# Kernel tuning notes

Hardware: AMD Instinct MI355X
Metric: run time of the kernel (lower is better)

The kernel has to match this reference:

```python
import jax, jax.numpy as jnp
import numpy as np

B, S, H = 32, 2048, 1024
STDV = 0.1


def setup_inputs() -> dict:
    key = jax.random.key(0)
    ks = jax.random.split(key, 8)
    u = lambda k, shape: jax.random.uniform(k, shape, minval=-STDV, maxval=STDV, dtype=jnp.float32)
    return {
        "inputs": jax.random.normal(ks[0], (B, S, H), dtype=jnp.float32),
        "qvector": jax.random.normal(ks[1], (B, H), dtype=jnp.float32),
        "W_u_1": u(ks[2], (H, H)),
        "W_u_m_1": u(ks[3], (H, H)),
        "W_u_h_1": u(ks[4], (H, 1)),
        "W_u_2": u(ks[5], (H, H)),
        "W_u_m_2": u(ks[6], (H, H)),
        "W_u_h_2": u(ks[7], (H, 1)),
    }


def reference(inputs, qvector, W_u_1, W_u_m_1, W_u_h_1, W_u_2, W_u_m_2, W_u_h_2):
    # inputs: [B, S, H], qvector: [B, H]
    def hop(m, W, Wm, Wh):
        # M = tanh(inputs @ W) gated by tanh(m @ Wm)  -> [B, S, H]
        M = jnp.tanh(jnp.einsum("bsh,hd->bsd", inputs, W))
        M = M * jnp.tanh(m @ Wm)[:, None, :]
        U = jnp.einsum("bsd,do->bso", M, Wh)        # [B, S, 1]
        alpha = jax.nn.softmax(U, axis=1)           # softmax over sequence
        return jnp.sum(inputs * alpha, axis=1)      # [B, H]

    mean_in = jnp.mean(inputs, axis=1)              # [B, H]
    u_att0 = mean_in
    m0 = mean_in * qvector
    u_att1 = hop(m0, W_u_1, W_u_m_1, W_u_h_1)
    m1 = m0 + u_att0 * qvector
    u_att2 = hop(m1, W_u_2, W_u_m_2, W_u_h_2)
    # original returns list [u_att0, u_att1, u_att2]; stack for a single array
    return jnp.stack([u_att0, u_att1, u_att2])      # [3, B, H]
```

## Files before the change

### kernel.cpp

```cpp
#include <hip/hip_runtime.h>
#include <hip/hip_bf16.h>
#include <math.h>

#define B_  32
#define S_  2048
#define H_  1024
#define M_TOT (B_ * S_)

typedef __bf16 bf16x8 __attribute__((ext_vector_type(8)));
typedef float  f32x4  __attribute__((ext_vector_type(4)));

__device__ __forceinline__ unsigned short f2bf(float f) {
    union { float f; unsigned int u; } v; v.f = f;
    unsigned int u = v.u;
    return (unsigned short)((u + 0x7fffu + ((u >> 16) & 1u)) >> 16);
}

__device__ __forceinline__ float bf2f(unsigned short s) {
    return __uint_as_float(((unsigned int)s) << 16);
}

__device__ __forceinline__ float fast_tanh(float x) {
    float e = __expf(2.0f * x);
    return 1.0f - 2.0f / (e + 1.0f);
}

__global__ void k_meanconv(const float* __restrict__ x,
                           unsigned short* __restrict__ xbf,
                           float* __restrict__ meanOut ) {
    int b  = blockIdx.x;
    int sc = blockIdx.y;
    int t  = threadIdx.x;
    size_t base = ((size_t)b * S_ + (size_t)sc * 32) * H_;
    const float4* xr = (const float4*)(x + base);
    ushort4* xo = (ushort4*)(xbf + base);
    float a0 = 0.f, a1 = 0.f, a2 = 0.f, a3 = 0.f;
    for (int s = 0; s < 32; ++s) {
        float4 v = xr[(size_t)s * 256 + t];
        a0 += v.x; a1 += v.y; a2 += v.z; a3 += v.w;
        ushort4 o;
        o.x = f2bf(v.x); o.y = f2bf(v.y); o.z = f2bf(v.z); o.w = f2bf(v.w);
        xo[(size_t)s * 256 + t] = o;
    }
    const float scl = 1.0f / (float)S_;
    float* mp = meanOut + b * H_ + t * 4;
    atomicAdd(mp + 0, a0 * scl);
    atomicAdd(mp + 1, a1 * scl);
    atomicAdd(mp + 2, a2 * scl);
    atomicAdd(mp + 3, a3 * scl);
}

__global__ void k_wconv(const float* __restrict__ W1,
                        const float* __restrict__ W2,
                        unsigned short* __restrict__ WT) {
    int n = blockIdx.x;
    int t = threadIdx.x;
    const float* src = (n < H_) ? (W1 + n) : (W2 + (n - H_));
    unsigned short* dst = WT + (size_t)n * H_;
    for (int kk = 0; kk < 4; ++kk) {
        int k = t + kk * 256;
        dst[k] = f2bf(src[(size_t)k * H_]);
    }
}

__global__ void k_vpart(const float* __restrict__ meanIn,
                        const float* __restrict__ q,
                        const float* __restrict__ Wm1,
                        const float* __restrict__ Wm2,
                        float* __restrict__ vtmp ) {
    int b   = blockIdx.x;
    int hop = blockIdx.y;
    int hc  = blockIdx.z;
    int t   = threadIdx.x;
    __shared__ float mL[128];
    float scale = (hop == 0) ? 1.0f : 2.0f;
    int h0 = hc * 128;
    if (t < 128)
        mL[t] = meanIn[b * H_ + h0 + t] * q[b * H_ + h0 + t] * scale;
    __syncthreads();
    const float* Wm = hop ? Wm2 : Wm1;
    int d0 = t * 4;
    float a0 = 0.f, a1 = 0.f, a2 = 0.f, a3 = 0.f;
    for (int h = 0; h < 128; ++h) {
        float m = mL[h];
        float4 w = *(const float4*)(Wm + (size_t)(h0 + h) * H_ + d0);
        a0 += m * w.x; a1 += m * w.y; a2 += m * w.z; a3 += m * w.w;
    }
    float* vo = vtmp + b * 2048 + hop * H_ + d0;
    atomicAdd(vo + 0, a0);
    atomicAdd(vo + 1, a1);
    atomicAdd(vo + 2, a2);
    atomicAdd(vo + 3, a3);
}

__global__ void k_vfin(const float* __restrict__ vtmp,
                       const float* __restrict__ Wh1,
                       const float* __restrict__ Wh2,
                       float* __restrict__ vcat) {
    int i = blockIdx.x * 256 + threadIdx.x;
    int hop = (i >> 10) & 1;
    int d = i & 1023;
    const float* Wh = hop ? Wh2 : Wh1;
    vcat[i] = tanhf(vtmp[i]) * Wh[d];
}

__global__ __launch_bounds__(256) void k_gemm(const unsigned short* __restrict__ Xbf,
                                              const unsigned short* __restrict__ WT,
                                              const float* __restrict__ vcat,
                                              float* __restrict__ U ) {
    int nt = blockIdx.x;
    int mt = blockIdx.y;
    int m0 = mt * 128;
    int n0 = nt * 128;
    int t    = threadIdx.x;
    int lane = t & 63;
    int wave = t >> 6;
    int wm = wave >> 1, wn = wave & 1;
    int fr = lane & 15;
    int fq = lane >> 4;

    __shared__ unsigned short As[128 * 32];
    __shared__ unsigned short Bs[128 * 32];

    f32x4 acc[4][4];
#pragma unroll
    for (int i = 0; i < 4; ++i)
#pragma unroll
        for (int j = 0; j < 4; ++j)
#pragma unroll
            for (int r = 0; r < 4; ++r) acc[i][j][r] = 0.0f;

    int idx0 = t, idx1 = t + 256;
    int row0 = idx0 >> 2, kc0 = ((idx0 & 3) - ((row0 >> 1) & 3)) & 3;
    int row1 = idx1 >> 2, kc1 = ((idx1 & 3) - ((row1 >> 1) & 3)) & 3;
    const unsigned short* gA0 = Xbf + (size_t)(m0 + row0) * H_ + kc0 * 8;
    const unsigned short* gA1 = Xbf + (size_t)(m0 + row1) * H_ + kc1 * 8;
    const unsigned short* gB0 = WT  + (size_t)(n0 + row0) * H_ + kc0 * 8;
    const unsigned short* gB1 = WT  + (size_t)(n0 + row1) * H_ + kc1 * 8;
    unsigned short* lA0 = As + idx0 * 8;
    unsigned short* lA1 = As + idx1 * 8;
    unsigned short* lB0 = Bs + idx0 * 8;
    unsigned short* lB1 = Bs + idx1 * 8;

    int slotR = (fq + ((fr >> 1) & 3)) & 3;
    const bf16x8* pa[4];
    const bf16x8* pb[4];
#pragma unroll
    for (int i = 0; i < 4; ++i)
        pa[i] = (const bf16x8*)(As + ((wm * 64 + i * 16 + fr) * 4 + slotR) * 8);
#pragma unroll
    for (int j = 0; j < 4; ++j)
        pb[j] = (const bf16x8*)(Bs + ((wn * 64 + j * 16 + fr) * 4 + slotR) * 8);

    for (int k0 = 0; k0 < H_; k0 += 32) {
        __builtin_amdgcn_global_load_lds((const __attribute__((address_space(1))) void*)(gA0 + k0),
                                         (__attribute__((address_space(3))) void*)lA0, 16, 0, 0);
        __builtin_amdgcn_global_load_lds((const __attribute__((address_space(1))) void*)(gA1 + k0),
                                         (__attribute__((address_space(3))) void*)lA1, 16, 0, 0);
        __builtin_amdgcn_global_load_lds((const __attribute__((address_space(1))) void*)(gB0 + k0),
                                         (__attribute__((address_space(3))) void*)lB0, 16, 0, 0);
        __builtin_amdgcn_global_load_lds((const __attribute__((address_space(1))) void*)(gB1 + k0),
                                         (__attribute__((address_space(3))) void*)lB1, 16, 0, 0);
        __syncthreads();
        bf16x8 af[4], bg[4];
#pragma unroll
        for (int i = 0; i < 4; ++i) af[i] = *pa[i];
#pragma unroll
        for (int j = 0; j < 4; ++j) bg[j] = *pb[j];
#pragma unroll
        for (int i = 0; i < 4; ++i)
#pragma unroll
            for (int j = 0; j < 4; ++j)
                acc[i][j] = __builtin_amdgcn_mfma_f32_16x16x32_bf16(af[i], bg[j], acc[i][j], 0, 0, 0);
        __syncthreads();
    }

    int b   = m0 >> 11;
    int hop = n0 >> 10;
    float vv[4];
#pragma unroll
    for (int j = 0; j < 4; ++j)
        vv[j] = vcat[b * 2048 + n0 + wn * 64 + j * 16 + fr];

#pragma unroll
    for (int i = 0; i < 4; ++i) {
#pragma unroll
        for (int r = 0; r < 4; ++r) {
            float sum = fast_tanh(acc[i][0][r]) * vv[0]
                      + fast_tanh(acc[i][1][r]) * vv[1]
                      + fast_tanh(acc[i][2][r]) * vv[2]
                      + fast_tanh(acc[i][3][r]) * vv[3];
            sum += __shfl_xor(sum, 1);
            sum += __shfl_xor(sum, 2);
            sum += __shfl_xor(sum, 4);
            sum += __shfl_xor(sum, 8);
            if (fr == 0) {
                int row = m0 + wm * 64 + i * 16 + fq * 4 + r;
                atomicAdd(&U[(size_t)hop * M_TOT + row], sum);
            }
        }
    }
}

__global__ void k_softmax(const float* __restrict__ U, float* __restrict__ alpha) {
    int id  = blockIdx.x;
    int hop = id >> 5, b = id & 31;
    int t = threadIdx.x;
    const float* u = U + (size_t)hop * M_TOT + (size_t)b * S_;
    float* al = alpha + (size_t)hop * M_TOT + (size_t)b * S_;
    float v[8];
    float mx = -1e30f;
#pragma unroll
    for (int i = 0; i < 8; ++i) { v[i] = u[t + i * 256]; mx = fmaxf(mx, v[i]); }
    __shared__ float red[256];
    red[t] = mx; __syncthreads();
    for (int s = 128; s > 0; s >>= 1) {
        if (t < s) red[t] = fmaxf(red[t], red[t + s]);
        __syncthreads();
    }
    mx = red[0]; __syncthreads();
    float sum = 0.f;
#pragma unroll
    for (int i = 0; i < 8; ++i) { v[i] = expf(v[i] - mx); sum += v[i]; }
    red[t] = sum; __syncthreads();
    for (int s = 128; s > 0; s >>= 1) {
        if (t < s) red[t] += red[t + s];
        __syncthreads();
    }
    float inv = 1.0f / red[0];
#pragma unroll
    for (int i = 0; i < 8; ++i) al[t + i * 256] = v[i] * inv;
}

__global__ void k_wsum(const unsigned short* __restrict__ Xbf,
                       const float* __restrict__ alpha,
                       float* __restrict__ out1 ,
                       float* __restrict__ out2 ) {
    int b  = blockIdx.x;
    int sc = blockIdx.y;
    int t  = threadIdx.x;
    __shared__ float a1[32], a2[32];
    int s0 = sc * 32;
    if (t < 32)       a1[t]      = alpha[(size_t)b * S_ + s0 + t];
    else if (t < 64)  a2[t - 32] = alpha[(size_t)M_TOT + (size_t)b * S_ + s0 + (t - 32)];
    __syncthreads();
    const ushort4* xr = (const ushort4*)(Xbf + ((size_t)b * S_ + s0) * H_);
    float x0a = 0.f, x1a = 0.f, x2a = 0.f, x3a = 0.f;
    float x0b = 0.f, x1b = 0.f, x2b = 0.f, x3b = 0.f;
    for (int s = 0; s < 32; ++s) {
        ushort4 u = xr[(size_t)s * 256 + t];
        float f0 = bf2f(u.x), f1 = bf2f(u.y), f2 = bf2f(u.z), f3 = bf2f(u.w);
        float w1 = a1[s], w2 = a2[s];
        x0a += f0 * w1; x1a += f1 * w1; x2a += f2 * w1; x3a += f3 * w1;
        x0b += f0 * w2; x1b += f1 * w2; x2b += f2 * w2; x3b += f3 * w2;
    }
    float* o1 = out1 + b * H_ + t * 4;
    float* o2 = out2 + b * H_ + t * 4;
    atomicAdd(o1 + 0, x0a); atomicAdd(o1 + 1, x1a);
    atomicAdd(o1 + 2, x2a); atomicAdd(o1 + 3, x3a);
    atomicAdd(o2 + 0, x0b); atomicAdd(o2 + 1, x1b);
    atomicAdd(o2 + 2, x2b); atomicAdd(o2 + 3, x3b);
}

extern "C" void kernel_launch(void* const* d_in, const int* in_sizes, int n_in,
                              void* d_out, int out_size, void* d_ws, size_t ws_size,
                              hipStream_t stream) {
    const float* inputs = (const float*)d_in[0];
    const float* q      = (const float*)d_in[1];
    const float* W1     = (const float*)d_in[2];
    const float* Wm1    = (const float*)d_in[3];
    const float* Wh1    = (const float*)d_in[4];
    const float* W2     = (const float*)d_in[5];
    const float* Wm2    = (const float*)d_in[6];
    const float* Wh2    = (const float*)d_in[7];
    float* out = (float*)d_out;

    char* ws = (char*)d_ws;
    unsigned short* Xbf  = (unsigned short*)(ws);
    unsigned short* WT   = (unsigned short*)(ws + 134217728);
    float*          vcat = (float*)(ws + 138412032);
    float*          U    = (float*)(ws + 138674176);
    float*          alph = (float*)(ws + 139198464);
    float*          vtmp = (float*)(ws + 139722752);

    hipMemsetAsync(d_out, 0, (size_t)out_size * sizeof(float), stream);
    hipMemsetAsync(U, 0, 524288 + 524288 + 262144, stream);

    k_meanconv<<<dim3(32, 64), 256, 0, stream>>>(inputs, Xbf, out);
    k_wconv  <<<dim3(2048),    256, 0, stream>>>(W1, W2, WT);
    k_vpart  <<<dim3(32, 2, 8), 256, 0, stream>>>(out, q, Wm1, Wm2, vtmp);
    k_vfin   <<<dim3(256),     256, 0, stream>>>(vtmp, Wh1, Wh2, vcat);
    k_gemm   <<<dim3(16, 512), 256, 0, stream>>>(Xbf, WT, vcat, U);
    k_softmax<<<dim3(64),      256, 0, stream>>>(U, alph);
    k_wsum   <<<dim3(32, 64),  256, 0, stream>>>(Xbf, alph, out + 32768, out + 65536);
}
```

Before: 870.0 us.

## Deepen GEMM K-tile to 64, tile weight transpose via LDS, widen wsum loads

The GEMM now stages 64-wide K slices in LDS with an 8-slot XOR-style swizzle, halving the number of barrier pairs per K loop, and adds a launch-bounds occupancy hint. The weight conversion kernel becomes a shared-memory tiled transpose with coalesced float4 reads and ushort4 writes, replacing strided column reads. The weighted-sum kernel uses 8-wide bf16 loads with 128 threads per block. Doubling the LDS footprint and the occupancy hint may cut resident blocks or force register spills.

```diff
diff --git a/kernel.cpp b/kernel.cpp
--- a/kernel.cpp
+++ b/kernel.cpp
@@ -9,6 +9,7 @@
 
 typedef __bf16 bf16x8 __attribute__((ext_vector_type(8)));
 typedef float  f32x4  __attribute__((ext_vector_type(4)));
+typedef unsigned short ushort8 __attribute__((ext_vector_type(8)));
 
 __device__ __forceinline__ unsigned short f2bf(float f) {
     union { float f; unsigned int u; } v; v.f = f;
@@ -53,13 +54,33 @@
 __global__ void k_wconv(const float* __restrict__ W1,
                         const float* __restrict__ W2,
                         unsigned short* __restrict__ WT) {
-    int n = blockIdx.x;
+    __shared__ float tile[64][65];
+    int kt = blockIdx.x * 64;
+    int nt = blockIdx.y * 64;
+    const float* W = blockIdx.z ? W2 : W1;
     int t = threadIdx.x;
-    const float* src = (n < H_) ? (W1 + n) : (W2 + (n - H_));
-    unsigned short* dst = WT + (size_t)n * H_;
-    for (int kk = 0; kk < 4; ++kk) {
-        int k = t + kk * 256;
-        dst[k] = f2bf(src[(size_t)k * H_]);
+    int r  = t >> 4;
+    int c4 = (t & 15) * 4;
+#pragma unroll
+    for (int i = 0; i < 4; ++i) {
+        float4 v = *(const float4*)(W + (size_t)(kt + r + i * 16) * H_ + nt + c4);
+        tile[r + i * 16][c4 + 0] = v.x;
+        tile[r + i * 16][c4 + 1] = v.y;
+        tile[r + i * 16][c4 + 2] = v.z;
+        tile[r + i * 16][c4 + 3] = v.w;
+    }
+    __syncthreads();
+    int n  = t & 63;
+    int kg = (t >> 6) * 16;
+    unsigned short* dst = WT + (size_t)(blockIdx.z * H_ + nt + n) * H_ + kt + kg;
+#pragma unroll
+    for (int jj = 0; jj < 4; ++jj) {
+        ushort4 o;
+        o.x = f2bf(tile[kg + jj * 4 + 0][n]);
+        o.y = f2bf(tile[kg + jj * 4 + 1][n]);
+        o.z = f2bf(tile[kg + jj * 4 + 2][n]);
+        o.w = f2bf(tile[kg + jj * 4 + 3][n]);
+        *(ushort4*)(dst + jj * 4) = o;
     }
 }
 
@@ -104,10 +125,10 @@
     vcat[i] = tanhf(vtmp[i]) * Wh[d];
 }
 
-__global__ __launch_bounds__(256) void k_gemm(const unsigned short* __restrict__ Xbf,
-                                              const unsigned short* __restrict__ WT,
-                                              const float* __restrict__ vcat,
-                                              float* __restrict__ U ) {
+__global__ __launch_bounds__(256, 5) void k_gemm(const unsigned short* __restrict__ Xbf,
+                                                 const unsigned short* __restrict__ WT,
+                                                 const float* __restrict__ vcat,
+                                                 float* __restrict__ U ) {
     int nt = blockIdx.x;
     int mt = blockIdx.y;
     int m0 = mt * 128;
@@ -119,8 +140,8 @@
     int fr = lane & 15;
     int fq = lane >> 4;
 
-    __shared__ unsigned short As[128 * 32];
-    __shared__ unsigned short Bs[128 * 32];
+    __shared__ unsigned short As[128 * 64];
+    __shared__ unsigned short Bs[128 * 64];
 
     f32x4 acc[4][4];
 #pragma unroll
@@ -130,48 +151,56 @@
 #pragma unroll
             for (int r = 0; r < 4; ++r) acc[i][j][r] = 0.0f;
 
-    int idx0 = t, idx1 = t + 256;
-    int row0 = idx0 >> 2, kc0 = ((idx0 & 3) - ((row0 >> 1) & 3)) & 3;
-    int row1 = idx1 >> 2, kc1 = ((idx1 & 3) - ((row1 >> 1) & 3)) & 3;
-    const unsigned short* gA0 = Xbf + (size_t)(m0 + row0) * H_ + kc0 * 8;
-    const unsigned short* gA1 = Xbf + (size_t)(m0 + row1) * H_ + kc1 * 8;
-    const unsigned short* gB0 = WT  + (size_t)(n0 + row0) * H_ + kc0 * 8;
-    const unsigned short* gB1 = WT  + (size_t)(n0 + row1) * H_ + kc1 * 8;
-    unsigned short* lA0 = As + idx0 * 8;
-    unsigned short* lA1 = As + idx1 * 8;
-    unsigned short* lB0 = Bs + idx0 * 8;
-    unsigned short* lB1 = Bs + idx1 * 8;
-
-    int slotR = (fq + ((fr >> 1) & 3)) & 3;
-    const bf16x8* pa[4];
-    const bf16x8* pb[4];
-#pragma unroll
-    for (int i = 0; i < 4; ++i)
-        pa[i] = (const bf16x8*)(As + ((wm * 64 + i * 16 + fr) * 4 + slotR) * 8);
-#pragma unroll
-    for (int j = 0; j < 4; ++j)
-        pb[j] = (const bf16x8*)(Bs + ((wn * 64 + j * 16 + fr) * 4 + slotR) * 8);
-
-    for (int k0 = 0; k0 < H_; k0 += 32) {
-        __builtin_amdgcn_global_load_lds((const __attribute__((address_space(1))) void*)(gA0 + k0),
-                                         (__attribute__((address_space(3))) void*)lA0, 16, 0, 0);
-        __builtin_amdgcn_global_load_lds((const __attribute__((address_space(1))) void*)(gA1 + k0),
-                                         (__attribute__((address_space(3))) void*)lA1, 16, 0, 0);
-        __builtin_amdgcn_global_load_lds((const __attribute__((address_space(1))) void*)(gB0 + k0),
-                                         (__attribute__((address_space(3))) void*)lB0, 16, 0, 0);
-        __builtin_amdgcn_global_load_lds((const __attribute__((address_space(1))) void*)(gB1 + k0),
-                                         (__attribute__((address_space(3))) void*)lB1, 16, 0, 0);
+    const unsigned short* gA[4];
+    const unsigned short* gB[4];
+    unsigned short* lA[4];
+    unsigned short* lB[4];
+#pragma unroll
+    for (int j = 0; j < 4; ++j) {
+        int idx = t + 256 * j;
+        int row = idx >> 3;
+        int kc  = ((idx & 7) - row) & 7;
+        gA[j] = Xbf + (size_t)(m0 + row) * H_ + kc * 8;
+        gB[j] = WT  + (size_t)(n0 + row) * H_ + kc * 8;
+        lA[j] = As + idx * 8;
+        lB[j] = Bs + idx * 8;
+    }
+
+    const bf16x8* pa[2][4];
+    const bf16x8* pb[2][4];
+#pragma unroll
+    for (int kk = 0; kk < 2; ++kk) {
+        int slot = ((kk * 4 + fq) + fr) & 7;
+#pragma unroll
+        for (int i = 0; i < 4; ++i)
+            pa[kk][i] = (const bf16x8*)(As + (wm * 64 + i * 16 + fr) * 64 + slot * 8);
+#pragma unroll
+        for (int j = 0; j < 4; ++j)
+            pb[kk][j] = (const bf16x8*)(Bs + (wn * 64 + j * 16 + fr) * 64 + slot * 8);
+    }
+
+    for (int k0 = 0; k0 < H_; k0 += 64) {
+#pragma unroll
+        for (int j = 0; j < 4; ++j) {
+            __builtin_amdgcn_global_load_lds((const __attribute__((address_space(1))) void*)(gA[j] + k0),
+                                             (__attribute__((address_space(3))) void*)lA[j], 16, 0, 0);
+            __builtin_amdgcn_global_load_lds((const __attribute__((address_space(1))) void*)(gB[j] + k0),
+                                             (__attribute__((address_space(3))) void*)lB[j], 16, 0, 0);
+        }
         __syncthreads();
-        bf16x8 af[4], bg[4];
-#pragma unroll
-        for (int i = 0; i < 4; ++i) af[i] = *pa[i];
-#pragma unroll
-        for (int j = 0; j < 4; ++j) bg[j] = *pb[j];
-#pragma unroll
-        for (int i = 0; i < 4; ++i)
-#pragma unroll
-            for (int j = 0; j < 4; ++j)
-                acc[i][j] = __builtin_amdgcn_mfma_f32_16x16x32_bf16(af[i], bg[j], acc[i][j], 0, 0, 0);
+#pragma unroll
+        for (int kk = 0; kk < 2; ++kk) {
+            bf16x8 af[4], bg[4];
+#pragma unroll
+            for (int i = 0; i < 4; ++i) af[i] = *pa[kk][i];
+#pragma unroll
+            for (int j = 0; j < 4; ++j) bg[j] = *pb[kk][j];
+#pragma unroll
+            for (int i = 0; i < 4; ++i)
+#pragma unroll
+                for (int j = 0; j < 4; ++j)
+                    acc[i][j] = __builtin_amdgcn_mfma_f32_16x16x32_bf16(af[i], bg[j], acc[i][j], 0, 0, 0);
+        }
         __syncthreads();
     }
 
@@ -244,22 +273,27 @@
     if (t < 32)       a1[t]      = alpha[(size_t)b * S_ + s0 + t];
     else if (t < 64)  a2[t - 32] = alpha[(size_t)M_TOT + (size_t)b * S_ + s0 + (t - 32)];
     __syncthreads();
-    const ushort4* xr = (const ushort4*)(Xbf + ((size_t)b * S_ + s0) * H_);
-    float x0a = 0.f, x1a = 0.f, x2a = 0.f, x3a = 0.f;
-    float x0b = 0.f, x1b = 0.f, x2b = 0.f, x3b = 0.f;
+    const ushort8* xr = (const ushort8*)(Xbf + ((size_t)b * S_ + s0) * H_);
+    float acc1[8], acc2[8];
+#pragma unroll
+    for (int e = 0; e < 8; ++e) { acc1[e] = 0.f; acc2[e] = 0.f; }
     for (int s = 0; s < 32; ++s) {
-        ushort4 u = xr[(size_t)s * 256 + t];
-        float f0 = bf2f(u.x), f1 = bf2f(u.y), f2 = bf2f(u.z), f3 = bf2f(u.w);
+        ushort8 u = xr[(size_t)s * 128 + t];
         float w1 = a1[s], w2 = a2[s];
-        x0a += f0 * w1; x1a += f1 * w1; x2a += f2 * w1; x3a += f3 * w1;
-        x0b += f0 * w2; x1b += f1 * w2; x2b += f2 * w2; x3b += f3 * w2;
-    }
-    float* o1 = out1 + b * H_ + t * 4;
-    float* o2 = out2 + b * H_ + t * 4;
-    atomicAdd(o1 + 0, x0a); atomicAdd(o1 + 1, x1a);
-    atomicAdd(o1 + 2, x2a); atomicAdd(o1 + 3, x3a);
-    atomicAdd(o2 + 0, x0b); atomicAdd(o2 + 1, x1b);
-    atomicAdd(o2 + 2, x2b); atomicAdd(o2 + 3, x3b);
+#pragma unroll
+        for (int e = 0; e < 8; ++e) {
+            float f = bf2f(u[e]);
+            acc1[e] += f * w1;
+            acc2[e] += f * w2;
+        }
+    }
+    float* o1 = out1 + b * H_ + t * 8;
+    float* o2 = out2 + b * H_ + t * 8;
+#pragma unroll
+    for (int e = 0; e < 8; ++e) {
+        atomicAdd(o1 + e, acc1[e]);
+        atomicAdd(o2 + e, acc2[e]);
+    }
 }
 
 extern "C" void kernel_launch(void* const* d_in, const int* in_sizes, int n_in,
@@ -286,11 +320,11 @@
     hipMemsetAsync(d_out, 0, (size_t)out_size * sizeof(float), stream);
     hipMemsetAsync(U, 0, 524288 + 524288 + 262144, stream);
 
-    k_meanconv<<<dim3(32, 64), 256, 0, stream>>>(inputs, Xbf, out);
-    k_wconv  <<<dim3(2048),    256, 0, stream>>>(W1, W2, WT);
-    k_vpart  <<<dim3(32, 2, 8), 256, 0, stream>>>(out, q, Wm1, Wm2, vtmp);
-    k_vfin   <<<dim3(256),     256, 0, stream>>>(vtmp, Wh1, Wh2, vcat);
-    k_gemm   <<<dim3(16, 512), 256, 0, stream>>>(Xbf, WT, vcat, U);
-    k_softmax<<<dim3(64),      256, 0, stream>>>(U, alph);
-    k_wsum   <<<dim3(32, 64),  256, 0, stream>>>(Xbf, alph, out + 32768, out + 65536);
-}
+    k_meanconv<<<dim3(32, 64),    256, 0, stream>>>(inputs, Xbf, out);
+    k_wconv  <<<dim3(16, 16, 2),  256, 0, stream>>>(W1, W2, WT);
+    k_vpart  <<<dim3(32, 2, 8),   256, 0, stream>>>(out, q, Wm1, Wm2, vtmp);
+    k_vfin   <<<dim3(256),        256, 0, stream>>>(vtmp, Wh1, Wh2, vcat);
+    k_gemm   <<<dim3(16, 512),    256, 0, stream>>>(Xbf, WT, vcat, U);
+    k_softmax<<<dim3(64),         256, 0, stream>>>(U, alph);
+    k_wsum   <<<dim3(32, 64),     128, 0, stream>>>(Xbf, alph, out + 32768, out + 65536);
+}
```

Measured after the change: 1.820 ms. 109% more time.
